# Performance work log

Hardware: AMD Instinct MI355X
Metric: run time of the kernel (lower is better)

## Reference

```python
import jax, jax.numpy as jnp
import numpy as np

N_HEADS = 8
EMBED_DIM = 512
HEAD_DIM = EMBED_DIM // N_HEADS
INPUT_DIM = 512


def setup_inputs() -> dict:
    key = jax.random.key(0)
    ks = jax.random.split(key, 9)
    B, N = 4, 2048
    s_in = 1.0 / np.sqrt(INPUT_DIM)
    s_e = 1.0 / np.sqrt(EMBED_DIM)
    return {
        "q": jax.random.normal(ks[0], (B, N, INPUT_DIM), dtype=jnp.float32),
        "wq": jax.random.uniform(ks[1], (EMBED_DIM, INPUT_DIM), jnp.float32, -s_in, s_in),
        "bq": jax.random.uniform(ks[2], (EMBED_DIM,), jnp.float32, -s_in, s_in),
        "wk": jax.random.uniform(ks[3], (EMBED_DIM, INPUT_DIM), jnp.float32, -s_in, s_in),
        "bk": jax.random.uniform(ks[4], (EMBED_DIM,), jnp.float32, -s_in, s_in),
        "wv": jax.random.uniform(ks[5], (EMBED_DIM, INPUT_DIM), jnp.float32, -s_in, s_in),
        "bv": jax.random.uniform(ks[6], (EMBED_DIM,), jnp.float32, -s_in, s_in),
        "wo": jax.random.uniform(ks[7], (EMBED_DIM, EMBED_DIM), jnp.float32, -s_e, s_e),
        "bo": jax.random.uniform(ks[8], (EMBED_DIM,), jnp.float32, -s_e, s_e),
    }


def reference(q, wq, bq, wk, bk, wv, bv, wo, bo):
    B, N, _ = q.shape
    # linear projections (torch Linear: x @ W.T + b)
    Q = (q @ wq.T + bq).reshape(B, N, N_HEADS, HEAD_DIM).transpose(0, 2, 1, 3)
    K = (q @ wk.T + bk).reshape(B, N, N_HEADS, HEAD_DIM).transpose(0, 2, 1, 3)
    V = (q @ wv.T + bv).reshape(B, N, N_HEADS, HEAD_DIM).transpose(0, 2, 1, 3)
    scores = jnp.einsum("bhqd,bhkd->bhqk", Q, K) / jnp.sqrt(
        jnp.asarray(HEAD_DIM, dtype=q.dtype)
    )
    weights = jax.nn.softmax(scores, axis=-1)
    out = jnp.einsum("bhqk,bhkd->bhqd", weights, V)  # [B,H,N,Dh]
    out = out.transpose(0, 2, 1, 3).reshape(B, N, EMBED_DIM)
    return out @ wo.T + bo
```

## Files before the change

### kernel.cpp

```cpp
#include <hip/hip_runtime.h>
#include <hip/hip_bf16.h>
#include <math.h>

#define SEQ    2048
#define DH     64
#define EMB    512
#define INDIM  512
#define NHEADS 8
#define BATCH  4
#define MTOT   (BATCH * SEQ)

typedef __attribute__((ext_vector_type(8))) short bf16x8;
typedef __attribute__((ext_vector_type(4))) float f32x4;

__device__ __forceinline__ ushort f2bf(float x) {
  union { float f; unsigned u; } v; v.f = x;
  unsigned r = v.u + 0x7FFFu + ((v.u >> 16) & 1u);
  return (ushort)(r >> 16);
}

__device__ __forceinline__ unsigned cvt_pk_bf16(float lo, float hi) {
  unsigned r;
  asm("v_cvt_pk_bf16_f32 %0, %1, %2" : "=v"(r) : "v"(lo), "v"(hi));
  return r;
}

__device__ __forceinline__ float fast_exp2(float x) {
  float r;
  asm("v_exp_f32 %0, %1" : "=v"(r) : "v"(x));
  return r;
}

__device__ __forceinline__ void permswap32(unsigned &x, unsigned &y) {
  asm("v_permlane32_swap_b32 %0, %1" : "+v"(x), "+v"(y));
}

__global__ __launch_bounds__(256) void conv_all(
    const float* __restrict__ x, const float* __restrict__ w0,
    const float* __restrict__ w1, const float* __restrict__ w2,
    const float* __restrict__ w3,
    ushort* __restrict__ dstX, ushort* __restrict__ dstW,
    int nX, int nW) {
  const int i = blockIdx.x * 256 + threadIdx.x;
  const float* src;
  ushort* dst;
  int idx;
  if (i < nX) {
    src = x; dst = dstX; idx = i;
  } else {
    const int j = i - nX;
    const int w = j / nW;
    idx = j - w * nW;
    src = (w == 0) ? w0 : (w == 1) ? w1 : (w == 2) ? w2 : w3;
    dst = dstW + (size_t)w * nW * 8;
  }
  const float4 a = ((const float4*)src)[idx * 2];
  const float4 b = ((const float4*)src)[idx * 2 + 1];
  uint4 o;
  o.x = cvt_pk_bf16(a.x, a.y);
  o.y = cvt_pk_bf16(a.z, a.w);
  o.z = cvt_pk_bf16(b.x, b.y);
  o.w = cvt_pk_bf16(b.z, b.w);
  ((uint4*)dst)[idx] = o;
}

template <int MODE>
__global__ __launch_bounds__(256) void mfma_gemm(
    const ushort* __restrict__ A, const ushort* __restrict__ W,
    const float* __restrict__ b0, const float* __restrict__ b1,
    const float* __restrict__ b2,
    ushort* __restrict__ outQ, ushort* __restrict__ outK,
    ushort* __restrict__ outVT, float* __restrict__ outF) {
  constexpr int BM = (MODE == 0) ? 128 : 64;
  constexpr int MF = (MODE == 0) ? 4 : 2;
  __shared__ __align__(16) char smem[MODE == 0 ? 35840 : 12288];
  ushort* As = (ushort*)smem;
  ushort* Bs = (ushort*)(smem + (MODE == 0 ? 8192 : 4096));
  ushort* Tl = (ushort*)smem;
  ushort* Tl2 = (ushort*)smem;

  const int bm = blockIdx.x * BM;
  const int bn = blockIdx.y * 128;
  const int tid = threadIdx.x;
  const int wave = tid >> 6, lane = tid & 63;
  const int g = lane >> 4, ln = lane & 15;
  const int wr = wave >> 1, wc = wave & 1;

  f32x4 acc[MF][4];
#pragma unroll
  for (int m = 0; m < MF; ++m)
#pragma unroll
    for (int n = 0; n < 4; ++n) acc[m][n] = (f32x4){0.f, 0.f, 0.f, 0.f};

  const size_t a_base = (size_t)(bm + wave * 16 + (lane >> 2)) * INDIM + (lane & 3) * 8;
  const size_t b_base = (size_t)(bn + wave * 16 + (lane >> 2)) * INDIM + (lane & 3) * 8;
  ushort* ldsA0 = As + wave * 512;
  ushort* ldsA1 = As + 2048 + wave * 512;
  ushort* ldsB0 = Bs + wave * 512;
  ushort* ldsB1 = Bs + 2048 + wave * 512;

  for (int k0 = 0; k0 < INDIM; k0 += 32) {
    __syncthreads();
    __builtin_amdgcn_global_load_lds(
        (const __attribute__((address_space(1))) void*)(A + a_base + k0),
        (__attribute__((address_space(3))) void*)ldsA0, 16, 0, 0);
    if (MODE == 0)
      __builtin_amdgcn_global_load_lds(
          (const __attribute__((address_space(1))) void*)(A + a_base + 64 * INDIM + k0),
          (__attribute__((address_space(3))) void*)ldsA1, 16, 0, 0);
    __builtin_amdgcn_global_load_lds(
        (const __attribute__((address_space(1))) void*)(W + b_base + k0),
        (__attribute__((address_space(3))) void*)ldsB0, 16, 0, 0);
    __builtin_amdgcn_global_load_lds(
        (const __attribute__((address_space(1))) void*)(W + b_base + 64 * INDIM + k0),
        (__attribute__((address_space(3))) void*)ldsB1, 16, 0, 0);
    __syncthreads();

    bf16x8 af[MF], bfv[4];
#pragma unroll
    for (int m = 0; m < MF; ++m)
      af[m] = *(const bf16x8*)&As[((MODE == 0 ? 64 : 32) * wr + 16 * m + ln) * 32 + 8 * g];
#pragma unroll
    for (int n = 0; n < 4; ++n)
      bfv[n] = *(const bf16x8*)&Bs[(64 * wc + 16 * n + ln) * 32 + 8 * g];
#pragma unroll
    for (int m = 0; m < MF; ++m)
#pragma unroll
      for (int n = 0; n < 4; ++n)
        acc[m][n] = __builtin_amdgcn_mfma_f32_16x16x32_bf16(af[m], bfv[n], acc[m][n], 0, 0, 0);
  }

  if (MODE == 1) {
#pragma unroll
    for (int n = 0; n < 4; ++n) {
      const int e = bn + 64 * wc + 16 * n + ln;
      const float bv = b0[e];
#pragma unroll
      for (int m = 0; m < MF; ++m)
#pragma unroll
        for (int r = 0; r < 4; ++r) {
          const int row = bm + 32 * wr + 16 * m + 4 * g + r;
          outF[(size_t)row * EMB + e] = acc[m][n][r] + bv;
        }
    }
    return;
  }

  const int which = bn >> 9;
  const float* bias = (which == 0) ? b0 : (which == 1) ? b1 : b2;

  if (which < 2) {
    const float scl = (which == 0) ? 0.18033688f : 1.0f;
    ushort* dst = (which == 0) ? outQ : outK;
    __syncthreads();
#pragma unroll
    for (int n = 0; n < 4; ++n) {
      const int cl = 64 * wc + 16 * n + ln;
      const float bv = bias[(bn & 511) + cl];
#pragma unroll
      for (int m = 0; m < 4; ++m)
#pragma unroll
        for (int r = 0; r < 4; ++r) {
          const int rl = 64 * wr + 16 * m + 4 * g + r;
          Tl2[rl * 136 + cl] = f2bf((acc[m][n][r] + bv) * scl);
        }
    }
    __syncthreads();
#pragma unroll
    for (int j = 0; j < 8; ++j) {
      const int cid = j * 256 + tid;
      const int seg = cid >> 3;
      const int l8 = cid & 7;
      const int rl = seg >> 1, half = seg & 1;
      const int row = bm + rl;
      const int b = row >> 11, nn = row & (SEQ - 1);
      const int h = ((bn & 511) >> 6) + half;
      const bf16x8 v = *(const bf16x8*)&Tl2[rl * 136 + half * 64 + l8 * 8];
      *(bf16x8*)&dst[(((size_t)(b * NHEADS + h) * SEQ) + nn) * DH + l8 * 8] = v;
    }
  } else {
    __syncthreads();
#pragma unroll
    for (int n = 0; n < 4; ++n) {
      const int cl = 64 * wc + 16 * n + ln;
      const float bv = bias[(bn & 511) + cl];
#pragma unroll
      for (int m = 0; m < 4; ++m)
#pragma unroll
        for (int r = 0; r < 4; ++r) {
          const int rl = 64 * wr + 16 * m + 4 * g + r;
          Tl[cl * 140 + rl] = f2bf(acc[m][n][r] + bv);
        }
    }
    __syncthreads();
    const int c = tid >> 1;
    const int rh = (tid & 1) * 64;
    const int e = (bn & 511) + c;
    const int h = e >> 6, d = e & 63;
    const int b = bm >> 11;
    const int nn0 = (bm & (SEQ - 1)) + rh;
    ushort* drow = outVT + (((size_t)(b * NHEADS + h) * DH) + d) * SEQ + nn0;
#pragma unroll
    for (int j = 0; j < 8; ++j)
      *(bf16x8*)&drow[j * 8] = *(const bf16x8*)&Tl[c * 140 + rh + j * 8];
  }
}

__global__ __launch_bounds__(512, 2) void attn_mfma(const ushort* __restrict__ Q,
                                                    const ushort* __restrict__ K,
                                                    const ushort* __restrict__ VT,
                                                    ushort* __restrict__ O) {
  __shared__ __align__(16) ushort Kl[2][2][64 * 72];
  __shared__ __align__(16) ushort Vl[2][2][64 * 72];

  const int tid = threadIdx.x;
  const int half = tid >> 8;
  const int ltid = tid & 255;
  const int wave = ltid >> 6, lane = ltid & 63;
  const int g = lane >> 4, ln = lane & 15;

  const int orig = blockIdx.x;
  const int swz = (orig & 7) * 64 + (orig >> 3);
  const int bh = swz >> 4;
  const int qx = swz & 15;
  const int qbase = qx * 128 + wave * 32;
  const int kvbase = half << 10;

  const ushort* Qb = Q + ((size_t)bh * SEQ + qbase) * DH;
  const ushort* Kb = K + (size_t)bh * SEQ * DH;
  const ushort* Vb = VT + (size_t)bh * DH * SEQ;

  const bf16x8 qfA0 = *(const bf16x8*)&Qb[ln * DH + 8 * g];
  const bf16x8 qfA1 = *(const bf16x8*)&Qb[ln * DH + 32 + 8 * g];
  const bf16x8 qfB0 = *(const bf16x8*)&Qb[(16 + ln) * DH + 8 * g];
  const bf16x8 qfB1 = *(const bf16x8*)&Qb[(16 + ln) * DH + 32 + 8 * g];

  bf16x8 vones;
#pragma unroll
  for (int i = 0; i < 8; ++i) vones[i] = (short)0x3F80;

  f32x4 oaccA[4], oaccB[4];
  f32x4 oaccDA = (f32x4){0.f, 0.f, 0.f, 0.f};
  f32x4 oaccDB = (f32x4){0.f, 0.f, 0.f, 0.f};
#pragma unroll
  for (int t = 0; t < 4; ++t) {
    oaccA[t] = (f32x4){0.f, 0.f, 0.f, 0.f};
    oaccB[t] = (f32x4){0.f, 0.f, 0.f, 0.f};
  }

  const int skv = ltid >> 3, sd = (ltid & 7) * 8;
  const int dt = ltid >> 2, kc = (ltid & 3) * 8;
  const int pr0 = skv ^ (((((skv >> 2) ^ (skv >> 3)) & 1)) * 12);
  const int s32 = skv + 32;
  const int pr1 = s32 ^ (((((s32 >> 2) ^ (s32 >> 3)) & 1)) * 12);

  bf16x8 k0v = *(const bf16x8*)&Kb[(size_t)(kvbase + skv) * DH + sd];
  bf16x8 k1v = *(const bf16x8*)&Kb[(size_t)(kvbase + 32 + skv) * DH + sd];
  bf16x8 v0v = *(const bf16x8*)&Vb[(size_t)dt * SEQ + kvbase + kc];
  bf16x8 v1v = *(const bf16x8*)&Vb[(size_t)dt * SEQ + kvbase + 32 + kc];
  *(bf16x8*)&Kl[half][0][pr0 * 72 + sd] = k0v;
  *(bf16x8*)&Kl[half][0][pr1 * 72 + sd] = k1v;
  *(bf16x8*)&Vl[half][0][dt * 72 + kc] = v0v;
  *(bf16x8*)&Vl[half][0][dt * 72 + 32 + kc] = v1v;
  k0v = *(const bf16x8*)&Kb[(size_t)(kvbase + 64 + skv) * DH + sd];
  k1v = *(const bf16x8*)&Kb[(size_t)(kvbase + 96 + skv) * DH + sd];
  v0v = *(const bf16x8*)&Vb[(size_t)dt * SEQ + kvbase + 64 + kc];
  v1v = *(const bf16x8*)&Vb[(size_t)dt * SEQ + kvbase + 96 + kc];
  asm volatile("s_waitcnt lgkmcnt(0)" ::: "memory");
  __builtin_amdgcn_s_barrier();

  for (int it = 0; it < 16; ++it) {
    const int cur = it & 1;
    const ushort* Kc = Kl[half][cur];
    const ushort* Vc = Vl[half][cur];

    if (it < 15) {
      ushort* Kn = Kl[half][cur ^ 1];
      ushort* Vn = Vl[half][cur ^ 1];
      *(bf16x8*)&Kn[pr0 * 72 + sd] = k0v;
      *(bf16x8*)&Kn[pr1 * 72 + sd] = k1v;
      *(bf16x8*)&Vn[dt * 72 + kc] = v0v;
      *(bf16x8*)&Vn[dt * 72 + 32 + kc] = v1v;
    }
    {
      const int nxt = kvbase + ((it + 2 < 16) ? (it + 2) * 64 : 15 * 64);
      k0v = *(const bf16x8*)&Kb[(size_t)(nxt + skv) * DH + sd];
      k1v = *(const bf16x8*)&Kb[(size_t)(nxt + 32 + skv) * DH + sd];
      v0v = *(const bf16x8*)&Vb[(size_t)dt * SEQ + nxt + kc];
      v1v = *(const bf16x8*)&Vb[(size_t)dt * SEQ + nxt + 32 + kc];
    }

    bf16x8 ka[4][2], vb[2][4];
#pragma unroll
    for (int t = 0; t < 4; ++t) {
      ka[t][0] = *(const bf16x8*)&Kc[(16 * t + ln) * 72 + 8 * g];
      ka[t][1] = *(const bf16x8*)&Kc[(16 * t + ln) * 72 + 32 + 8 * g];
    }
#pragma unroll
    for (int c = 0; c < 2; ++c)
#pragma unroll
      for (int t = 0; t < 4; ++t)
        vb[c][t] = *(const bf16x8*)&Vc[(16 * t + ln) * 72 + 32 * c + 8 * g];

    f32x4 sA0 = (f32x4){0.f, 0.f, 0.f, 0.f};
    f32x4 sA1 = sA0, sA2 = sA0, sA3 = sA0;
    f32x4 sB0 = sA0, sB1 = sA0, sB2 = sA0, sB3 = sA0;
    __builtin_amdgcn_s_setprio(1);
    sA0 = __builtin_amdgcn_mfma_f32_16x16x32_bf16(ka[0][0], qfA0, sA0, 0, 0, 0);
    sB0 = __builtin_amdgcn_mfma_f32_16x16x32_bf16(ka[0][0], qfB0, sB0, 0, 0, 0);
    sA1 = __builtin_amdgcn_mfma_f32_16x16x32_bf16(ka[1][0], qfA0, sA1, 0, 0, 0);
    sB1 = __builtin_amdgcn_mfma_f32_16x16x32_bf16(ka[1][0], qfB0, sB1, 0, 0, 0);
    sA2 = __builtin_amdgcn_mfma_f32_16x16x32_bf16(ka[2][0], qfA0, sA2, 0, 0, 0);
    sB2 = __builtin_amdgcn_mfma_f32_16x16x32_bf16(ka[2][0], qfB0, sB2, 0, 0, 0);
    sA3 = __builtin_amdgcn_mfma_f32_16x16x32_bf16(ka[3][0], qfA0, sA3, 0, 0, 0);
    sB3 = __builtin_amdgcn_mfma_f32_16x16x32_bf16(ka[3][0], qfB0, sB3, 0, 0, 0);
    sA0 = __builtin_amdgcn_mfma_f32_16x16x32_bf16(ka[0][1], qfA1, sA0, 0, 0, 0);
    sB0 = __builtin_amdgcn_mfma_f32_16x16x32_bf16(ka[0][1], qfB1, sB0, 0, 0, 0);
    sA1 = __builtin_amdgcn_mfma_f32_16x16x32_bf16(ka[1][1], qfA1, sA1, 0, 0, 0);
    sB1 = __builtin_amdgcn_mfma_f32_16x16x32_bf16(ka[1][1], qfB1, sB1, 0, 0, 0);
    sA2 = __builtin_amdgcn_mfma_f32_16x16x32_bf16(ka[2][1], qfA1, sA2, 0, 0, 0);
    sB2 = __builtin_amdgcn_mfma_f32_16x16x32_bf16(ka[2][1], qfB1, sB2, 0, 0, 0);
    sA3 = __builtin_amdgcn_mfma_f32_16x16x32_bf16(ka[3][1], qfA1, sA3, 0, 0, 0);
    sB3 = __builtin_amdgcn_mfma_f32_16x16x32_bf16(ka[3][1], qfB1, sB3, 0, 0, 0);
    __builtin_amdgcn_s_setprio(0);

    float pA0[4], pA1[4], pA2[4], pA3[4];
    float pB0[4], pB1[4], pB2[4], pB3[4];
#pragma unroll
    for (int r = 0; r < 4; ++r) {
      pA0[r] = fast_exp2(sA0[r]);
      pA1[r] = fast_exp2(sA1[r]);
      pA2[r] = fast_exp2(sA2[r]);
      pA3[r] = fast_exp2(sA3[r]);
      pB0[r] = fast_exp2(sB0[r]);
      pB1[r] = fast_exp2(sB1[r]);
      pB2[r] = fast_exp2(sB2[r]);
      pB3[r] = fast_exp2(sB3[r]);
    }

    unsigned aa0 = cvt_pk_bf16(pA0[0], pA0[1]);
    unsigned aa2 = cvt_pk_bf16(pA1[0], pA1[1]);
    unsigned aa1 = cvt_pk_bf16(pA0[2], pA0[3]);
    unsigned aa3 = cvt_pk_bf16(pA1[2], pA1[3]);
    permswap32(aa0, aa2);
    permswap32(aa1, aa3);
    unsigned ab0 = cvt_pk_bf16(pA2[0], pA2[1]);
    unsigned ab2 = cvt_pk_bf16(pA3[0], pA3[1]);
    unsigned ab1 = cvt_pk_bf16(pA2[2], pA2[3]);
    unsigned ab3 = cvt_pk_bf16(pA3[2], pA3[3]);
    permswap32(ab0, ab2);
    permswap32(ab1, ab3);
    unsigned ba0 = cvt_pk_bf16(pB0[0], pB0[1]);
    unsigned ba2 = cvt_pk_bf16(pB1[0], pB1[1]);
    unsigned ba1 = cvt_pk_bf16(pB0[2], pB0[3]);
    unsigned ba3 = cvt_pk_bf16(pB1[2], pB1[3]);
    permswap32(ba0, ba2);
    permswap32(ba1, ba3);
    unsigned bb0 = cvt_pk_bf16(pB2[0], pB2[1]);
    unsigned bb2 = cvt_pk_bf16(pB3[0], pB3[1]);
    unsigned bb1 = cvt_pk_bf16(pB2[2], pB2[3]);
    unsigned bb3 = cvt_pk_bf16(pB3[2], pB3[3]);
    permswap32(bb0, bb2);
    permswap32(bb1, bb3);
    union { unsigned u[4]; bf16x8 v; } paA0, paA1, paB0, paB1;
    paA0.u[0] = aa0; paA0.u[1] = aa1; paA0.u[2] = aa2; paA0.u[3] = aa3;
    paA1.u[0] = ab0; paA1.u[1] = ab1; paA1.u[2] = ab2; paA1.u[3] = ab3;
    paB0.u[0] = ba0; paB0.u[1] = ba1; paB0.u[2] = ba2; paB0.u[3] = ba3;
    paB1.u[0] = bb0; paB1.u[1] = bb1; paB1.u[2] = bb2; paB1.u[3] = bb3;

    __builtin_amdgcn_s_setprio(1);
#pragma unroll
    for (int t = 0; t < 4; ++t) {
      oaccA[t] = __builtin_amdgcn_mfma_f32_16x16x32_bf16(paA0.v, vb[0][t], oaccA[t], 0, 0, 0);
      oaccB[t] = __builtin_amdgcn_mfma_f32_16x16x32_bf16(paB0.v, vb[0][t], oaccB[t], 0, 0, 0);
      oaccA[t] = __builtin_amdgcn_mfma_f32_16x16x32_bf16(paA1.v, vb[1][t], oaccA[t], 0, 0, 0);
      oaccB[t] = __builtin_amdgcn_mfma_f32_16x16x32_bf16(paB1.v, vb[1][t], oaccB[t], 0, 0, 0);
    }
    oaccDA = __builtin_amdgcn_mfma_f32_16x16x32_bf16(paA0.v, vones, oaccDA, 0, 0, 0);
    oaccDB = __builtin_amdgcn_mfma_f32_16x16x32_bf16(paB0.v, vones, oaccDB, 0, 0, 0);
    oaccDA = __builtin_amdgcn_mfma_f32_16x16x32_bf16(paA1.v, vones, oaccDA, 0, 0, 0);
    oaccDB = __builtin_amdgcn_mfma_f32_16x16x32_bf16(paB1.v, vones, oaccDB, 0, 0, 0);
    __builtin_amdgcn_s_setprio(0);

    asm volatile("s_waitcnt lgkmcnt(0)" ::: "memory");
    __builtin_amdgcn_s_barrier();
  }

  float* Acc = (float*)&Kl[0][0][0];
  float* Dl  = (float*)&Vl[0][0][0];
  __syncthreads();
  if (half == 0) {
#pragma unroll
    for (int t = 0; t < 4; ++t)
#pragma unroll
      for (int r = 0; r < 4; ++r) {
        Acc[(wave * 32 + 4 * g + r) * 68 + 16 * t + ln] = oaccA[t][r];
        Acc[(wave * 32 + 16 + 4 * g + r) * 68 + 16 * t + ln] = oaccB[t][r];
      }
    if (ln == 0) {
#pragma unroll
      for (int r = 0; r < 4; ++r) {
        Dl[wave * 32 + 4 * g + r] = oaccDA[r];
        Dl[wave * 32 + 16 + 4 * g + r] = oaccDB[r];
      }
    }
  }
  __syncthreads();
  if (half == 1) {
    const int b = bh >> 3, h = bh & 7;
#pragma unroll
    for (int r = 0; r < 4; ++r) {
      const int rowA = wave * 32 + 4 * g + r;
      const int rowB = rowA + 16;
      const float irA = 1.0f / (Dl[rowA] + oaccDA[r]);
      const float irB = 1.0f / (Dl[rowB] + oaccDB[r]);
      ushort* opA = O + ((size_t)(b * SEQ) + qx * 128 + rowA) * EMB + h * 64;
      ushort* opB = O + ((size_t)(b * SEQ) + qx * 128 + rowB) * EMB + h * 64;
#pragma unroll
      for (int t = 0; t < 4; ++t) {
        opA[16 * t + ln] = f2bf((Acc[rowA * 68 + 16 * t + ln] + oaccA[t][r]) * irA);
        opB[16 * t + ln] = f2bf((Acc[rowB * 68 + 16 * t + ln] + oaccB[t][r]) * irB);
      }
    }
  }
}

extern "C" void kernel_launch(void* const* d_in, const int* in_sizes, int n_in,
                              void* d_out, int out_size, void* d_ws, size_t ws_size,
                              hipStream_t stream) {
  const float* q  = (const float*)d_in[0];
  const float* wq = (const float*)d_in[1];
  const float* bq = (const float*)d_in[2];
  const float* wk = (const float*)d_in[3];
  const float* bk = (const float*)d_in[4];
  const float* wv = (const float*)d_in[5];
  const float* bv = (const float*)d_in[6];
  const float* wo = (const float*)d_in[7];
  const float* bo = (const float*)d_in[8];
  float* out = (float*)d_out;

  const size_t XSZ = (size_t)MTOT * INDIM;
  const size_t WSZ = (size_t)EMB * INDIM;
  const size_t QSZ = (size_t)BATCH * NHEADS * SEQ * DH;
  ushort* wsX = (ushort*)d_ws;
  ushort* wsW = wsX + XSZ;
  ushort* wsQ = wsW + 4 * WSZ;
  ushort* wsK = wsQ + QSZ;
  ushort* wsVT = wsK + QSZ;
  ushort* wsA = wsVT + QSZ;

  const dim3 blk(256);

  const int nX = (int)(XSZ / 8);
  const int nW = (int)(WSZ / 8);
  conv_all<<<dim3((nX + 4 * nW) / 256), blk, 0, stream>>>(
      q, wq, wk, wv, wo, wsX, wsW, nX, nW);

  mfma_gemm<0><<<dim3(MTOT / 128, 1536 / 128), blk, 0, stream>>>(
      wsX, wsW, bq, bk, bv, wsQ, wsK, wsVT, nullptr);

  attn_mfma<<<dim3(512), dim3(512), 0, stream>>>(wsQ, wsK, wsVT, wsA);

  mfma_gemm<1><<<dim3(MTOT / 64, EMB / 128), blk, 0, stream>>>(
      wsA, wsW + 3 * WSZ, bo, nullptr, nullptr, nullptr, nullptr, nullptr, out);
}
```

Measured before the change: 96.18 us.

## Single-buffer K/V shared tiles in attention kernel to halve LDS footprint

```diff
diff --git a/kernel.cpp b/kernel.cpp
--- a/kernel.cpp
+++ b/kernel.cpp
@@ -210,14 +210,16 @@
                                                     const ushort* __restrict__ K,
                                                     const ushort* __restrict__ VT,
                                                     ushort* __restrict__ O) {
-  __shared__ __align__(16) ushort Kl[2][2][64 * 72];
-  __shared__ __align__(16) ushort Vl[2][2][64 * 72];
+  __shared__ __align__(16) char smem[36864];
 
   const int tid = threadIdx.x;
   const int half = tid >> 8;
   const int ltid = tid & 255;
   const int wave = ltid >> 6, lane = ltid & 63;
   const int g = lane >> 4, ln = lane & 15;
+
+  ushort* Kh = (ushort*)(smem + half * 9216);
+  ushort* Vh = (ushort*)(smem + 18432 + half * 9216);
 
   const int orig = blockIdx.x;
   const int swz = (orig & 7) * 64 + (orig >> 3);
@@ -258,49 +260,36 @@
   bf16x8 k1v = *(const bf16x8*)&Kb[(size_t)(kvbase + 32 + skv) * DH + sd];
   bf16x8 v0v = *(const bf16x8*)&Vb[(size_t)dt * SEQ + kvbase + kc];
   bf16x8 v1v = *(const bf16x8*)&Vb[(size_t)dt * SEQ + kvbase + 32 + kc];
-  *(bf16x8*)&Kl[half][0][pr0 * 72 + sd] = k0v;
-  *(bf16x8*)&Kl[half][0][pr1 * 72 + sd] = k1v;
-  *(bf16x8*)&Vl[half][0][dt * 72 + kc] = v0v;
-  *(bf16x8*)&Vl[half][0][dt * 72 + 32 + kc] = v1v;
-  k0v = *(const bf16x8*)&Kb[(size_t)(kvbase + 64 + skv) * DH + sd];
-  k1v = *(const bf16x8*)&Kb[(size_t)(kvbase + 96 + skv) * DH + sd];
-  v0v = *(const bf16x8*)&Vb[(size_t)dt * SEQ + kvbase + 64 + kc];
-  v1v = *(const bf16x8*)&Vb[(size_t)dt * SEQ + kvbase + 96 + kc];
-  asm volatile("s_waitcnt lgkmcnt(0)" ::: "memory");
-  __builtin_amdgcn_s_barrier();
 
   for (int it = 0; it < 16; ++it) {
-    const int cur = it & 1;
-    const ushort* Kc = Kl[half][cur];
-    const ushort* Vc = Vl[half][cur];
-
-    if (it < 15) {
-      ushort* Kn = Kl[half][cur ^ 1];
-      ushort* Vn = Vl[half][cur ^ 1];
-      *(bf16x8*)&Kn[pr0 * 72 + sd] = k0v;
-      *(bf16x8*)&Kn[pr1 * 72 + sd] = k1v;
-      *(bf16x8*)&Vn[dt * 72 + kc] = v0v;
-      *(bf16x8*)&Vn[dt * 72 + 32 + kc] = v1v;
-    }
+    __syncthreads();
+    *(bf16x8*)&Kh[pr0 * 72 + sd] = k0v;
+    *(bf16x8*)&Kh[pr1 * 72 + sd] = k1v;
+    *(bf16x8*)&Vh[dt * 72 + kc] = v0v;
+    *(bf16x8*)&Vh[dt * 72 + 32 + kc] = v1v;
+
     {
-      const int nxt = kvbase + ((it + 2 < 16) ? (it + 2) * 64 : 15 * 64);
+      const int nxt = kvbase + ((it + 1 < 16) ? (it + 1) * 64 : 15 * 64);
       k0v = *(const bf16x8*)&Kb[(size_t)(nxt + skv) * DH + sd];
       k1v = *(const bf16x8*)&Kb[(size_t)(nxt + 32 + skv) * DH + sd];
       v0v = *(const bf16x8*)&Vb[(size_t)dt * SEQ + nxt + kc];
       v1v = *(const bf16x8*)&Vb[(size_t)dt * SEQ + nxt + 32 + kc];
     }
 
+    asm volatile("s_waitcnt lgkmcnt(0)" ::: "memory");
+    __builtin_amdgcn_s_barrier();
+
     bf16x8 ka[4][2], vb[2][4];
 #pragma unroll
     for (int t = 0; t < 4; ++t) {
-      ka[t][0] = *(const bf16x8*)&Kc[(16 * t + ln) * 72 + 8 * g];
-      ka[t][1] = *(const bf16x8*)&Kc[(16 * t + ln) * 72 + 32 + 8 * g];
+      ka[t][0] = *(const bf16x8*)&Kh[(16 * t + ln) * 72 + 8 * g];
+      ka[t][1] = *(const bf16x8*)&Kh[(16 * t + ln) * 72 + 32 + 8 * g];
     }
 #pragma unroll
     for (int c = 0; c < 2; ++c)
 #pragma unroll
       for (int t = 0; t < 4; ++t)
-        vb[c][t] = *(const bf16x8*)&Vc[(16 * t + ln) * 72 + 32 * c + 8 * g];
+        vb[c][t] = *(const bf16x8*)&Vh[(16 * t + ln) * 72 + 32 * c + 8 * g];
 
     f32x4 sA0 = (f32x4){0.f, 0.f, 0.f, 0.f};
     f32x4 sA1 = sA0, sA2 = sA0, sA3 = sA0;
@@ -381,13 +370,10 @@
     oaccDA = __builtin_amdgcn_mfma_f32_16x16x32_bf16(paA1.v, vones, oaccDA, 0, 0, 0);
     oaccDB = __builtin_amdgcn_mfma_f32_16x16x32_bf16(paB1.v, vones, oaccDB, 0, 0, 0);
     __builtin_amdgcn_s_setprio(0);
-
-    asm volatile("s_waitcnt lgkmcnt(0)" ::: "memory");
-    __builtin_amdgcn_s_barrier();
-  }
-
-  float* Acc = (float*)&Kl[0][0][0];
-  float* Dl  = (float*)&Vl[0][0][0];
+  }
+
+  float* Acc = (float*)smem;
+  float* Dl  = (float*)(smem + 34816);
   __syncthreads();
   if (half == 0) {
 #pragma unroll
```

After: 94.53 us, median of 2. About the same (-1.7%).
